# Kernel optimization log

Hardware: AMD Instinct MI355X
Metric: run time of the kernel (lower is better)

## Reference

```python
import jax, jax.numpy as jnp
import numpy as np

D_MODEL = 1024
D_STATE = 256

def setup_inputs() -> dict:
    key = jax.random.key(0)
    k1, k2, k3, k4 = jax.random.split(key, 4)
    x = jax.random.normal(k1, (8, 4096, D_MODEL), dtype=jnp.float32)
    A = jax.random.normal(k2, (D_STATE,), dtype=jnp.float32)
    B = jax.random.normal(k3, (D_STATE, D_MODEL), dtype=jnp.float32) * 0.01
    C = jax.random.normal(k4, (D_MODEL, D_STATE), dtype=jnp.float32) * 0.01
    D = jnp.ones((D_MODEL,), dtype=jnp.float32)
    return {"x": x, "A": A, "B": B, "C": C, "D": D}

def reference(x, A, B, C, D):
    # x: (b, s, d_model)
    a_bar = jnp.exp(-jnp.exp(A))                     # (n,)
    Bx = jnp.einsum('bsd,nd->bsn', x, B)             # (b, s, n) precomputed input drive

    def step(h, bx_t):
        h = a_bar * h + bx_t                          # (b, n)
        return h, h

    h0 = jnp.zeros((x.shape[0], A.shape[0]), dtype=x.dtype)
    # scan over time axis: move seq to leading axis
    _, hs = jax.lax.scan(step, h0, jnp.swapaxes(Bx, 0, 1))  # hs: (s, b, n)
    hs = jnp.swapaxes(hs, 0, 1)                      # (b, s, n)
    y = jnp.einsum('bsn,dn->bsd', hs, C) + D * x     # (b, s, d_model)
    return y
```

## Files before the change

### kernel.cpp

```cpp
#include <hip/hip_runtime.h>
#include <cstdint>
#include <cstddef>


typedef __attribute__((ext_vector_type(8))) _Float16 half8;
typedef __attribute__((ext_vector_type(4))) float f32x4;

__device__ inline half8 cvt8(float4 a, float4 b) {
  half8 h;
  h[0] = (_Float16)a.x; h[1] = (_Float16)a.y;
  h[2] = (_Float16)a.z; h[3] = (_Float16)a.w;
  h[4] = (_Float16)b.x; h[5] = (_Float16)b.y;
  h[6] = (_Float16)b.z; h[7] = (_Float16)b.w;
  return h;
}

__global__ __launch_bounds__(256) void cvt_bc(
    const float* __restrict__ Bp, const float* __restrict__ Cp,
    _Float16* __restrict__ Bh, _Float16* __restrict__ Ch)
{
  const int g = blockIdx.x * 256 + threadIdx.x;
  const size_t off = (size_t)(g & 32767) * 8;
  const float* src = (g < 32768) ? (Bp + off) : (Cp + off);
  _Float16*    dst = (g < 32768) ? (Bh + off) : (Ch + off);
  float4 a = *(const float4*)src;
  float4 b = *(const float4*)(src + 4);
  *(half8*)dst = cvt8(a, b);
}

__global__ __launch_bounds__(256) void gemm_bx(
    const float* __restrict__ x, const _Float16* __restrict__ Bh,
    const float* __restrict__ Ap,
    _Float16* __restrict__ Bxh, float* __restrict__ E)
{
  __shared__ _Float16 lb[256 * 128];

  const int tid  = threadIdx.x;
  const int lane = tid & 63;
  const int wave = tid >> 6;
  const int quad = lane >> 4;
  const int l16  = lane & 15;
  const long blockM = (long)blockIdx.x * 64;
  const long arow = blockM + wave * 16 + l16;

  f32x4 acc[16];
  #pragma unroll
  for (int i = 0; i < 16; i++) acc[i] = (f32x4){0.f, 0.f, 0.f, 0.f};

  for (int kc = 0; kc < 8; kc++) {
    __syncthreads();
    {
      const int n = tid;
      const _Float16* src = Bh + (size_t)n * 1024 + kc * 128;
      #pragma unroll
      for (int j = 0; j < 16; j++) {
        half8 v = *(const half8*)(src + j * 8);
        const int k8p = j ^ (n & 7);
        *(half8*)&lb[n * 128 + k8p * 8] = v;
      }
    }
    half8 af[4];
    #pragma unroll
    for (int ks = 0; ks < 4; ks++) {
      const float* ga = x + arow * 1024 + kc * 128 + ks * 32 + quad * 8;
      float4 a0 = *(const float4*)ga;
      float4 a1 = *(const float4*)(ga + 4);
      af[ks] = cvt8(a0, a1);
    }
    __syncthreads();
    #pragma unroll
    for (int ks = 0; ks < 4; ks++) {
      #pragma unroll
      for (int nt = 0; nt < 16; nt++) {
        const int n   = nt * 16 + l16;
        const int k8p = (ks * 4 + quad) ^ (n & 7);
        half8 bf = *(const half8*)&lb[n * 128 + k8p * 8];
        acc[nt] = __builtin_amdgcn_mfma_f32_16x16x32_f16(af[ks], bf, acc[nt], 0, 0, 0);
      }
    }
  }

  __syncthreads();
  #pragma unroll
  for (int nt = 0; nt < 16; nt++)
    #pragma unroll
    for (int r = 0; r < 4; r++)
      lb[(wave * 16 + quad * 4 + r) * 256 + nt * 16 + l16] = (_Float16)acc[nt][r];
  __syncthreads();
  {
    const int row = tid >> 2, seg = tid & 3;
    _Float16* dst = Bxh + (blockM + row) * 256 + seg * 64;
    const _Float16* srcl = &lb[row * 256 + seg * 64];
    #pragma unroll
    for (int j = 0; j < 8; j++)
      *(half8*)(dst + j * 8) = *(const half8*)(srcl + j * 8);
  }
  {
    const float al = expf(-expf(Ap[tid]));
    float h = 0.f;
    #pragma unroll 8
    for (int t = 0; t < 64; t++)
      h = fmaf(al, h, (float)lb[t * 256 + tid]);
    E[(size_t)blockIdx.x * 256 + tid] = h;
  }
}

__global__ __launch_bounds__(256) void scan_prefix(
    const float* __restrict__ E, const float* __restrict__ Ap,
    float* __restrict__ carry)
{
  __shared__ float4 se4[4096];
  const int n = threadIdx.x;
  const int b = blockIdx.x;

  const float4* src4 = (const float4*)(E + (size_t)b * 64 * 256);
  #pragma unroll
  for (int j = 0; j < 16; j++)
    se4[j * 256 + n] = src4[j * 256 + n];

  const float al = expf(-expf(Ap[n]));
  float aL = al;
  #pragma unroll
  for (int i = 0; i < 6; i++) aL *= aL;

  __syncthreads();
  const float* se = (const float*)se4;
  float run = 0.f;
  for (int c = 0; c < 64; c++) {
    carry[((size_t)b * 64 + c) * 256 + n] = run;
    run = fmaf(aL, run, se[c * 256 + n]);
  }
}

__global__ __launch_bounds__(256) void scan_apply(
    _Float16* __restrict__ Bxh, const float* __restrict__ Ap,
    const float* __restrict__ carry)
{
  const int n  = threadIdx.x;
  const int bc = blockIdx.x;
  const float al = expf(-expf(Ap[n]));
  float h = carry[(size_t)bc * 256 + n];
  const size_t base = (size_t)bc * 64 * 256 + n;
  #pragma unroll 16
  for (int t = 0; t < 64; t++) {
    const size_t i = base + (size_t)t * 256;
    h = fmaf(al, h, (float)Bxh[i]);
    Bxh[i] = (_Float16)h;
  }
}

__global__ __launch_bounds__(256, 4) void gemm_y(
    const _Float16* __restrict__ hs, const _Float16* __restrict__ Ch,
    const float* __restrict__ x, const float* __restrict__ Dp,
    float* __restrict__ y)
{
  __shared__ _Float16 lc[64 * 256];

  const int tid  = threadIdx.x;
  const int lane = tid & 63;
  const int wave = tid >> 6;
  const int quad = lane >> 4;
  const int l16  = lane & 15;
  const int slab = blockIdx.x & 15;
  const int mg   = blockIdx.x >> 4;
  const int n0   = slab * 64;

  {
    const int n = tid >> 2, q = tid & 3;
    const _Float16* src = Ch + (size_t)(n0 + n) * 256 + q * 64;
    #pragma unroll
    for (int j = 0; j < 8; j++) {
      half8 v = *(const half8*)(src + j * 8);
      const int k8p = (q * 8 + j) ^ (n & 7);
      *(half8*)&lc[n * 256 + k8p * 8] = v;
    }
  }

  float dv[4];
  #pragma unroll
  for (int nt = 0; nt < 4; nt++) dv[nt] = Dp[n0 + nt * 16 + l16];

  __syncthreads();

  for (int i = 0; i < 4; i++) {
    const long chunk   = (long)mg * 4 + i;
    const long rowbase = chunk * 64 + wave * 16;

    half8 af[8];
    #pragma unroll
    for (int ks = 0; ks < 8; ks++)
      af[ks] = *(const half8*)(hs + (rowbase + l16) * 256 + ks * 32 + quad * 8);

    float xv[4][4];
    #pragma unroll
    for (int r = 0; r < 4; r++) {
      const float* gx = x + (rowbase + quad * 4 + r) * 1024 + n0 + l16;
      #pragma unroll
      for (int nt = 0; nt < 4; nt++) xv[r][nt] = gx[nt * 16];
    }

    f32x4 acc[4];
    #pragma unroll
    for (int nt = 0; nt < 4; nt++) acc[nt] = (f32x4){0.f, 0.f, 0.f, 0.f};

    #pragma unroll
    for (int ks = 0; ks < 8; ks++) {
      #pragma unroll
      for (int nt = 0; nt < 4; nt++) {
        const int n   = nt * 16 + l16;
        const int k8p = (ks * 4 + quad) ^ (n & 7);
        half8 bf = *(const half8*)&lc[n * 256 + k8p * 8];
        acc[nt] = __builtin_amdgcn_mfma_f32_16x16x32_f16(af[ks], bf, acc[nt], 0, 0, 0);
      }
    }

    #pragma unroll
    for (int r = 0; r < 4; r++) {
      float* gy = y + (rowbase + quad * 4 + r) * 1024 + n0 + l16;
      #pragma unroll
      for (int nt = 0; nt < 4; nt++)
        gy[nt * 16] = acc[nt][r] + dv[nt] * xv[r][nt];
    }
  }
}

extern "C" void kernel_launch(void* const* d_in, const int* in_sizes, int n_in,
                              void* d_out, int out_size, void* d_ws, size_t ws_size,
                              hipStream_t stream) {
  const float* x  = (const float*)d_in[0];
  const float* Ap = (const float*)d_in[1];
  const float* Bp = (const float*)d_in[2];
  const float* Cp = (const float*)d_in[3];
  const float* Dp = (const float*)d_in[4];
  float* y = (float*)d_out;

  _Float16* Bxh = (_Float16*)d_ws;
  _Float16* Bh  = Bxh + (size_t)32768 * 256;
  _Float16* Ch  = Bh + (size_t)256 * 1024;
  float* E      = (float*)(Ch + (size_t)1024 * 256);
  float* carry  = E + (size_t)512 * 256;

  cvt_bc     <<<256,  256, 0, stream>>>(Bp, Cp, Bh, Ch);
  gemm_bx    <<<512,  256, 0, stream>>>(x, Bh, Ap, Bxh, E);
  scan_prefix<<<8,    256, 0, stream>>>(E, Ap, carry);
  scan_apply <<<512,  256, 0, stream>>>(Bxh, Ap, carry);
  gemm_y     <<<2048, 256, 0, stream>>>(Bxh, Ch, x, Dp, y);
}
```

Measured before the change: 334.6 us.

## Double-buffer gemm_y chunk loads and transpose MFMA for float4 epilogue

Swaps the MFMA operand order in gemm_y so each lane holds four consecutive output columns. The x reads, D reads and y writes then become float4 vector accesses instead of scalar strided ones. The four row chunks are software-pipelined with two register buffers, so the next chunk's hs and x loads are issued before the current chunk's MFMAs. The extra register pressure is handled by lowering the launch-bounds occupancy hint from 4 to 3 blocks.

```diff
diff --git a/kernel.cpp b/kernel.cpp
--- a/kernel.cpp
+++ b/kernel.cpp
@@ -149,7 +149,7 @@
   }
 }
 
-__global__ __launch_bounds__(256, 4) void gemm_y(
+__global__ __launch_bounds__(256, 3) void gemm_y(
     const _Float16* __restrict__ hs, const _Float16* __restrict__ Ch,
     const float* __restrict__ x, const float* __restrict__ Dp,
     float* __restrict__ y)
@@ -175,30 +175,22 @@
       *(half8*)&lc[n * 256 + k8p * 8] = v;
     }
   }
-
-  float dv[4];
-  #pragma unroll
-  for (int nt = 0; nt < 4; nt++) dv[nt] = Dp[n0 + nt * 16 + l16];
-
-  __syncthreads();
-
-  for (int i = 0; i < 4; i++) {
-    const long chunk   = (long)mg * 4 + i;
-    const long rowbase = chunk * 64 + wave * 16;
-
-    half8 af[8];
+  __syncthreads();
+
+  auto load_chunk = [&](int i, half8* af, float4* xv) {
+    const long row = ((long)mg * 4 + i) * 64 + wave * 16 + l16;
+    const _Float16* ph = hs + row * 256;
     #pragma unroll
     for (int ks = 0; ks < 8; ks++)
-      af[ks] = *(const half8*)(hs + (rowbase + l16) * 256 + ks * 32 + quad * 8);
-
-    float xv[4][4];
-    #pragma unroll
-    for (int r = 0; r < 4; r++) {
-      const float* gx = x + (rowbase + quad * 4 + r) * 1024 + n0 + l16;
-      #pragma unroll
-      for (int nt = 0; nt < 4; nt++) xv[r][nt] = gx[nt * 16];
-    }
-
+      af[ks] = *(const half8*)(ph + ks * 32 + quad * 8);
+    const float* px = x + row * 1024 + n0 + quad * 4;
+    #pragma unroll
+    for (int nt = 0; nt < 4; nt++)
+      xv[nt] = *(const float4*)(px + nt * 16);
+  };
+
+  auto compute_chunk = [&](int i, const half8* af, const float4* xv) {
+    const long row = ((long)mg * 4 + i) * 64 + wave * 16 + l16;
     f32x4 acc[4];
     #pragma unroll
     for (int nt = 0; nt < 4; nt++) acc[nt] = (f32x4){0.f, 0.f, 0.f, 0.f};
@@ -209,19 +201,35 @@
       for (int nt = 0; nt < 4; nt++) {
         const int n   = nt * 16 + l16;
         const int k8p = (ks * 4 + quad) ^ (n & 7);
-        half8 bf = *(const half8*)&lc[n * 256 + k8p * 8];
-        acc[nt] = __builtin_amdgcn_mfma_f32_16x16x32_f16(af[ks], bf, acc[nt], 0, 0, 0);
+        half8 cf = *(const half8*)&lc[n * 256 + k8p * 8];
+        acc[nt] = __builtin_amdgcn_mfma_f32_16x16x32_f16(cf, af[ks], acc[nt], 0, 0, 0);
       }
     }
 
-    #pragma unroll
-    for (int r = 0; r < 4; r++) {
-      float* gy = y + (rowbase + quad * 4 + r) * 1024 + n0 + l16;
-      #pragma unroll
-      for (int nt = 0; nt < 4; nt++)
-        gy[nt * 16] = acc[nt][r] + dv[nt] * xv[r][nt];
-    }
-  }
+    float* py = y + row * 1024 + n0 + quad * 4;
+    const float* pD = Dp + n0 + quad * 4;
+    #pragma unroll
+    for (int nt = 0; nt < 4; nt++) {
+      float4 dv = *(const float4*)(pD + nt * 16);
+      float4 o;
+      o.x = acc[nt][0] + dv.x * xv[nt].x;
+      o.y = acc[nt][1] + dv.y * xv[nt].y;
+      o.z = acc[nt][2] + dv.z * xv[nt].z;
+      o.w = acc[nt][3] + dv.w * xv[nt].w;
+      *(float4*)(py + nt * 16) = o;
+    }
+  };
+
+  half8 afA[8], afB[8];
+  float4 xvA[4], xvB[4];
+  load_chunk(0, afA, xvA);
+  load_chunk(1, afB, xvB);
+  compute_chunk(0, afA, xvA);
+  load_chunk(2, afA, xvA);
+  compute_chunk(1, afB, xvB);
+  load_chunk(3, afB, xvB);
+  compute_chunk(2, afA, xvA);
+  compute_chunk(3, afB, xvB);
 }
 
 extern "C" void kernel_launch(void* const* d_in, const int* in_sizes, int n_in,
```

Result: no change. 328.6 us (-1.8%).
